# Kernel optimization log

Hardware: AMD Instinct MI355X
Metric: run time of the kernel (lower is better)

The kernel has to match this reference:

```python
import jax, jax.numpy as jnp
import numpy as np

DEGREE = 4  # sh degree -> DEGREE**2 = 16 components
RES = 128
N_PTS = 2097152
CH = 3


def sh_components(degree, d):
    """Real SH basis values for unit directions d [..., 3] -> [..., degree**2]."""
    x, y, z = d[..., 0], d[..., 1], d[..., 2]
    xx, yy, zz = x * x, y * y, z * z
    xy, yz, xz = x * y, y * z, x * z
    comps = [jnp.full(x.shape, 0.28209479177387814, dtype=d.dtype)]
    if degree > 1:
        comps += [-0.4886025119029199 * y,
                  0.4886025119029199 * z,
                  -0.4886025119029199 * x]
    if degree > 2:
        comps += [1.0925484305920792 * xy,
                  -1.0925484305920792 * yz,
                  0.31539156525252005 * (2.0 * zz - xx - yy),
                  -1.0925484305920792 * xz,
                  0.5462742152960396 * (xx - yy)]
    if degree > 3:
        comps += [-0.5900435899266435 * y * (3 * xx - yy),
                  2.890611442640554 * xy * z,
                  -0.4570457994644658 * y * (4 * zz - xx - yy),
                  0.3731763325901154 * z * (2 * zz - 3 * xx - 3 * yy),
                  -0.4570457994644658 * x * (4 * zz - xx - yy),
                  1.445305721320277 * z * (xx - yy),
                  -0.5900435899266435 * x * (xx - 3 * yy)]
    if degree > 4:
        comps += [2.5033429417967046 * xy * (xx - yy),
                  -1.7701307697799304 * yz * (3 * xx - yy),
                  0.9461746957575601 * xy * (7 * zz - 1),
                  -0.6690465435572892 * yz * (7 * zz - 3),
                  0.10578554691520431 * (zz * (35 * zz - 30) + 3),
                  -0.6690465435572892 * xz * (7 * zz - 3),
                  0.47308734787878004 * (xx - yy) * (7 * zz - 1),
                  -1.7701307697799304 * xz * (xx - 3 * yy),
                  0.6258357354491761 * (xx * (xx - 3 * yy) - yy * (3 * xx - yy))]
    return jnp.stack(comps, axis=-1)


def trilerp(coefficients, aabb, points):
    """Trilinear interpolation of grid coefficients [R,R,R,D2,C] at points [N,3] -> [N,D2,C]."""
    res = coefficients.shape[0]
    amin, amax = aabb[:3], aabb[3:]
    g = (points - amin) / (amax - amin) * (res - 1)       # continuous grid coords
    g = jnp.clip(g, 0.0, res - 1.0)
    i0 = jnp.clip(jnp.floor(g).astype(jnp.int32), 0, res - 2)  # [N,3]
    f = g - i0.astype(g.dtype)                            # fractional part [N,3]
    fx, fy, fz = f[..., 0], f[..., 1], f[..., 2]
    out = None
    for dx in (0, 1):
        wx = fx if dx else (1.0 - fx)
        for dy in (0, 1):
            wy = fy if dy else (1.0 - fy)
            for dz in (0, 1):
                wz = fz if dz else (1.0 - fz)
                w = (wx * wy * wz)[:, None, None]          # [N,1,1]
                c = coefficients[i0[:, 0] + dx, i0[:, 1] + dy, i0[:, 2] + dz]  # [N,D2,C]
                out = w * c if out is None else out + w * c
    return out


def setup_inputs() -> dict:
    key = jax.random.key(0)
    k1, k2, k3 = jax.random.split(key, 3)
    coefficients = jax.random.normal(k1, (RES, RES, RES, DEGREE ** 2, CH), dtype=jnp.float32) * 0.1
    aabb = jnp.array([-1.0, -1.0, -1.0, 1.0, 1.0, 1.0], dtype=jnp.float32)
    points = jax.random.uniform(k2, (N_PTS, 3), dtype=jnp.float32) * 2.0 - 1.0  # inside aabb
    normals = jax.random.normal(k3, (N_PTS, 3), dtype=jnp.float32)
    normals = normals / jnp.linalg.norm(normals, axis=-1, keepdims=True)
    return {"coefficients": coefficients, "aabb": aabb, "points": points, "normals": normals}


def reference(coefficients, aabb, points, normals):
    comps = sh_components(DEGREE, normals)                 # [N, D2]
    ic = trilerp(coefficients, aabb, points)               # [N, D2, C]
    irradiance = jnp.sum(ic * comps[..., None], axis=1)    # [N, C]
    return jnp.maximum(irradiance, 0.0)
```

## Files before the change

kernel.cpp:

```cpp
#include <hip/hip_runtime.h>


constexpr int RES = 128;
constexpr int D2 = 16;
constexpr int CSTRIDE = D2 * 3;
constexpr int CELL_F4 = CSTRIDE / 4;

constexpr int NBX = 32, NBY = 16, NBZ = 16;
constexpr int NBINS = NBX * NBY * NBZ;
constexpr int HX = 5, HY = 9, HZ = 9;
constexpr int TOT_F4 = HX * HY * HZ * CELL_F4;
constexpr int MAIN_THREADS = 256;
constexpr int LOAD_ITERS = (TOT_F4 + MAIN_THREADS - 1) / MAIN_THREADS;
constexpr int PAD = 16;

__device__ __forceinline__ void grid_coords(const float* aabb, float px, float py, float pz,
                                            int& ix, int& iy, int& iz,
                                            float& fx, float& fy, float& fz)
{
    const float a0 = aabb[0], a1 = aabb[1], a2 = aabb[2];
    const float b0 = aabb[3], b1 = aabb[4], b2 = aabb[5];
    float gx = (px - a0) / (b0 - a0) * (float)(RES - 1);
    float gy = (py - a1) / (b1 - a1) * (float)(RES - 1);
    float gz = (pz - a2) / (b2 - a2) * (float)(RES - 1);
    gx = fminf(fmaxf(gx, 0.0f), (float)(RES - 1));
    gy = fminf(fmaxf(gy, 0.0f), (float)(RES - 1));
    gz = fminf(fmaxf(gz, 0.0f), (float)(RES - 1));
    ix = min((int)floorf(gx), RES - 2);
    iy = min((int)floorf(gy), RES - 2);
    iz = min((int)floorf(gz), RES - 2);
    fx = gx - (float)ix;
    fy = gy - (float)iy;
    fz = gz - (float)iz;
}

__device__ __forceinline__ int bin_of(int ix, int iy, int iz)
{
    return (((ix >> 2) * NBY) + (iy >> 3)) * NBZ + (iz >> 3);
}

__device__ __forceinline__ void sh_basis(float nx, float ny, float nz, float* sh)
{
    const float xx = nx * nx, yy = ny * ny, zz = nz * nz;
    const float xy = nx * ny, yz = ny * nz, xz = nx * nz;
    sh[0]  = 0.28209479177387814f;
    sh[1]  = -0.4886025119029199f * ny;
    sh[2]  = 0.4886025119029199f * nz;
    sh[3]  = -0.4886025119029199f * nx;
    sh[4]  = 1.0925484305920792f * xy;
    sh[5]  = -1.0925484305920792f * yz;
    sh[6]  = 0.31539156525252005f * (2.0f * zz - xx - yy);
    sh[7]  = -1.0925484305920792f * xz;
    sh[8]  = 0.5462742152960396f * (xx - yy);
    sh[9]  = -0.5900435899266435f * ny * (3.0f * xx - yy);
    sh[10] = 2.890611442640554f * xy * nz;
    sh[11] = -0.4570457994644658f * ny * (4.0f * zz - xx - yy);
    sh[12] = 0.3731763325901154f * nz * (2.0f * zz - 3.0f * xx - 3.0f * yy);
    sh[13] = -0.4570457994644658f * nx * (4.0f * zz - xx - yy);
    sh[14] = 1.445305721320277f * nz * (xx - yy);
    sh[15] = -0.5900435899266435f * nx * (xx - 3.0f * yy);
}

__global__ __launch_bounds__(256) void hist_kernel(
    const float* __restrict__ aabb,
    const float* __restrict__ points,
    int* __restrict__ bin_of_point,
    int* __restrict__ hist_p,
    int n)
{
    const int i = blockIdx.x * blockDim.x + threadIdx.x;
    if (i >= n) return;
    int ix, iy, iz; float fx, fy, fz;
    grid_coords(aabb, points[3 * i + 0], points[3 * i + 1], points[3 * i + 2],
                ix, iy, iz, fx, fy, fz);
    const int bin = bin_of(ix, iy, iz);
    bin_of_point[i] = bin;
    atomicAdd(&hist_p[bin * PAD], 1);
}

__global__ __launch_bounds__(256) void scan_kernel(
    const int* __restrict__ hist_p,
    int* __restrict__ binstart,
    int* __restrict__ cursor_p)
{
    __shared__ int lsum[256];
    const int t = threadIdx.x;
    constexpr int PER = NBINS / 256;
    const int base = t * PER;
    int loc[PER];
    int s = 0;
#pragma unroll
    for (int k = 0; k < PER; ++k) { loc[k] = hist_p[(base + k) * PAD]; s += loc[k]; }
    lsum[t] = s;
    __syncthreads();
    for (int off = 1; off < 256; off <<= 1) {
        int v = (t >= off) ? lsum[t - off] : 0;
        __syncthreads();
        lsum[t] += v;
        __syncthreads();
    }
    int run = lsum[t] - s;
#pragma unroll
    for (int k = 0; k < PER; ++k) {
        binstart[base + k] = run;
        cursor_p[(base + k) * PAD] = run;
        run += loc[k];
    }
}

__global__ __launch_bounds__(256) void scatter_kernel(
    const int* __restrict__ bin_of_point,
    int* __restrict__ cursor_p,
    int* __restrict__ sidx,
    int n)
{
    const int i = blockIdx.x * blockDim.x + threadIdx.x;
    if (i >= n) return;
    const int bin = bin_of_point[i];
    const int pos = atomicAdd(&cursor_p[bin * PAD], 1);
    sidx[pos] = i;
}

__global__ __launch_bounds__(MAIN_THREADS) void main_kernel(
    const float* __restrict__ coeff,
    const float* __restrict__ aabb,
    const float* __restrict__ points,
    const float* __restrict__ normals,
    const int* __restrict__ binstart,
    const int* __restrict__ hist_p,
    const int* __restrict__ sidx,
    float* __restrict__ out)
{
    extern __shared__ char smem[];
    float4* lds4 = (float4*)smem;

    const int bin = blockIdx.x;
    const int start = binstart[bin];
    const int count = hist_p[bin * PAD];
    if (count == 0) return;

    const int bx = bin / (NBY * NBZ);
    const int by = (bin / NBZ) % NBY;
    const int bz = bin % NBZ;
    const int x0 = bx << 2;
    const int y0 = by << 3;
    const int z0 = bz << 3;

    const int tid = threadIdx.x;
    const float4* __restrict__ coeff4 = (const float4*)coeff;

#pragma unroll
    for (int k = 0; k < LOAD_ITERS; ++k) {
        const int u = tid + k * MAIN_THREADS;
        if (u < TOT_F4) {
            int cx = u / (HY * HZ * CELL_F4);
            int r1 = u - cx * (HY * HZ * CELL_F4);
            int cy = r1 / (HZ * CELL_F4);
            int r2 = r1 - cy * (HZ * CELL_F4);
            int cz = r2 / CELL_F4;
            int kk = r2 - cz * CELL_F4;
            int xg = min(x0 + cx, RES - 1);
            int yg = min(y0 + cy, RES - 1);
            int zg = min(z0 + cz, RES - 1);
            lds4[u] = coeff4[((xg * RES + yg) * RES + zg) * CELL_F4 + kk];
        }
    }
    __syncthreads();

    for (int p = start + tid; p < start + count; p += MAIN_THREADS) {
        const int i = sidx[p];
        const float px = points[3 * i + 0];
        const float py = points[3 * i + 1];
        const float pz = points[3 * i + 2];
        const float nx = normals[3 * i + 0];
        const float ny = normals[3 * i + 1];
        const float nz = normals[3 * i + 2];

        int ix, iy, iz; float fx, fy, fz;
        grid_coords(aabb, px, py, pz, ix, iy, iz, fx, fy, fz);
        const int lx = ix - x0, ly = iy - y0, lz = iz - z0;

        float sh[D2];
        sh_basis(nx, ny, nz, sh);

        const float wz0 = 1.0f - fz, wz1 = fz;
        float acc0 = 0.0f, acc1 = 0.0f, acc2 = 0.0f;

#pragma unroll
        for (int dx = 0; dx < 2; ++dx) {
            const float wx = dx ? fx : 1.0f - fx;
#pragma unroll
            for (int dy = 0; dy < 2; ++dy) {
                const float wxy = wx * (dy ? fy : 1.0f - fy);
                const int lcell = (((lx + dx) * HY + (ly + dy)) * HZ + lz) * CELL_F4;
                union { float4 q[24]; float v[96]; } u;
#pragma unroll
                for (int kk = 0; kk < 24; ++kk) u.q[kk] = lds4[lcell + kk];

                float s00 = 0.f, s01 = 0.f, s02 = 0.f;
                float s10 = 0.f, s11 = 0.f, s12 = 0.f;
#pragma unroll
                for (int j = 0; j < D2; ++j) {
                    const float s = sh[j];
                    s00 = fmaf(s, u.v[3 * j + 0], s00);
                    s01 = fmaf(s, u.v[3 * j + 1], s01);
                    s02 = fmaf(s, u.v[3 * j + 2], s02);
                    s10 = fmaf(s, u.v[48 + 3 * j + 0], s10);
                    s11 = fmaf(s, u.v[48 + 3 * j + 1], s11);
                    s12 = fmaf(s, u.v[48 + 3 * j + 2], s12);
                }
                const float w0 = wxy * wz0, w1 = wxy * wz1;
                acc0 = fmaf(w0, s00, fmaf(w1, s10, acc0));
                acc1 = fmaf(w0, s01, fmaf(w1, s11, acc1));
                acc2 = fmaf(w0, s02, fmaf(w1, s12, acc2));
            }
        }

        out[3 * i + 0] = fmaxf(acc0, 0.0f);
        out[3 * i + 1] = fmaxf(acc1, 0.0f);
        out[3 * i + 2] = fmaxf(acc2, 0.0f);
    }
}

__global__ __launch_bounds__(256) void direct_kernel(
    const float* __restrict__ coeff,
    const float* __restrict__ aabb,
    const float* __restrict__ points,
    const float* __restrict__ normals,
    float* __restrict__ out,
    int n)
{
    const int i = blockIdx.x * blockDim.x + threadIdx.x;
    if (i >= n) return;
    const float px = points[3 * i + 0], py = points[3 * i + 1], pz = points[3 * i + 2];
    const float nx = normals[3 * i + 0], ny = normals[3 * i + 1], nz = normals[3 * i + 2];
    int ix, iy, iz; float fx, fy, fz;
    grid_coords(aabb, px, py, pz, ix, iy, iz, fx, fy, fz);
    float sh[D2];
    sh_basis(nx, ny, nz, sh);
    const float wz0 = 1.0f - fz, wz1 = fz;
    float acc0 = 0.0f, acc1 = 0.0f, acc2 = 0.0f;
#pragma unroll
    for (int dx = 0; dx < 2; ++dx) {
        const float wx = dx ? fx : 1.0f - fx;
#pragma unroll
        for (int dy = 0; dy < 2; ++dy) {
            const float wxy = wx * (dy ? fy : 1.0f - fy);
            const int cell = (((ix + dx) * RES + (iy + dy)) * RES + iz) * CSTRIDE;
            const float4* __restrict__ cp = (const float4*)(coeff + cell);
            union { float4 q[24]; float v[96]; } u;
#pragma unroll
            for (int kk = 0; kk < 24; ++kk) u.q[kk] = cp[kk];
            float s00 = 0.f, s01 = 0.f, s02 = 0.f;
            float s10 = 0.f, s11 = 0.f, s12 = 0.f;
#pragma unroll
            for (int j = 0; j < D2; ++j) {
                const float s = sh[j];
                s00 = fmaf(s, u.v[3 * j + 0], s00);
                s01 = fmaf(s, u.v[3 * j + 1], s01);
                s02 = fmaf(s, u.v[3 * j + 2], s02);
                s10 = fmaf(s, u.v[48 + 3 * j + 0], s10);
                s11 = fmaf(s, u.v[48 + 3 * j + 1], s11);
                s12 = fmaf(s, u.v[48 + 3 * j + 2], s12);
            }
            const float w0 = wxy * wz0, w1 = wxy * wz1;
            acc0 = fmaf(w0, s00, fmaf(w1, s10, acc0));
            acc1 = fmaf(w0, s01, fmaf(w1, s11, acc1));
            acc2 = fmaf(w0, s02, fmaf(w1, s12, acc2));
        }
    }
    out[3 * i + 0] = fmaxf(acc0, 0.0f);
    out[3 * i + 1] = fmaxf(acc1, 0.0f);
    out[3 * i + 2] = fmaxf(acc2, 0.0f);
}

extern "C" void kernel_launch(void* const* d_in, const int* in_sizes, int n_in,
                              void* d_out, int out_size, void* d_ws, size_t ws_size,
                              hipStream_t stream) {
    const float* coeff   = (const float*)d_in[0];
    const float* aabb    = (const float*)d_in[1];
    const float* points  = (const float*)d_in[2];
    const float* normals = (const float*)d_in[3];
    float* out = (float*)d_out;

    const int n = in_sizes[2] / 3;
    const int nblk = (n + 255) / 256;

    size_t off = 0;
    auto take = [&](size_t bytes) { size_t o = off; off = (off + bytes + 255) & ~(size_t)255; return o; };
    char* ws = (char*)d_ws;
    const size_t o_bin      = take((size_t)n * 4);
    const size_t o_hist     = take((size_t)NBINS * PAD * 4);
    const size_t o_binstart = take((size_t)NBINS * 4);
    const size_t o_cursor   = take((size_t)NBINS * PAD * 4);
    const size_t o_sidx     = take((size_t)n * 4);
    const size_t needed = off;

    if (ws_size < needed) {
        hipLaunchKernelGGL(direct_kernel, dim3(nblk), dim3(256), 0, stream,
                           coeff, aabb, points, normals, out, n);
        return;
    }

    int* bin_of_point = (int*)(ws + o_bin);
    int* hist_p   = (int*)(ws + o_hist);
    int* binstart = (int*)(ws + o_binstart);
    int* cursor_p = (int*)(ws + o_cursor);
    int* sidx     = (int*)(ws + o_sidx);

    hipMemsetAsync(hist_p, 0, (size_t)NBINS * PAD * 4, stream);

    hipLaunchKernelGGL(hist_kernel, dim3(nblk), dim3(256), 0, stream,
                       aabb, points, bin_of_point, hist_p, n);
    hipLaunchKernelGGL(scan_kernel, dim3(1), dim3(256), 0, stream,
                       hist_p, binstart, cursor_p);
    hipLaunchKernelGGL(scatter_kernel, dim3(nblk), dim3(256), 0, stream,
                       bin_of_point, cursor_p, sidx, n);
    hipLaunchKernelGGL(main_kernel, dim3(NBINS), dim3(MAIN_THREADS),
                       TOT_F4 * sizeof(float4), stream,
                       coeff, aabb, points, normals, binstart, hist_p, sidx, out);
}
```

Before: 922.5 us.

## Replace histogram-scan-scatter binning with fixed-capacity replicated bin slots

Drops the separate histogram, prefix-scan and scatter passes and instead writes each point index straight into one of four replicated fixed-capacity slot arrays per spatial bin in a single pass. Spreading each bin over four counters is meant to reduce contention on the atomics. Points that do not fit go to an overflow list, which a new overflow kernel handles through global-memory gathers. A rare fallback that scans every point if the overflow list itself fills is also included. This removes one pass over the points and the serial single-block scan, at the cost of an extra kernel launch and a capacity-dependent overflow path.

Result: faster. 828.3 us (-10.2%).

```diff
diff --git a/kernel.cpp b/kernel.cpp
--- a/kernel.cpp
+++ b/kernel.cpp
@@ -12,7 +12,11 @@
 constexpr int TOT_F4 = HX * HY * HZ * CELL_F4;
 constexpr int MAIN_THREADS = 256;
 constexpr int LOAD_ITERS = (TOT_F4 + MAIN_THREADS - 1) / MAIN_THREADS;
-constexpr int PAD = 16;
+
+constexpr int REPL = 4;
+constexpr int CAP = 104;
+constexpr int CNT_PAD = 16;
+constexpr int OVF_CAP = 131072;
 
 __device__ __forceinline__ void grid_coords(const float* aabb, float px, float py, float pz,
                                             int& ix, int& iy, int& iz,
@@ -61,11 +65,62 @@
     sh[15] = -0.5900435899266435f * nx * (xx - 3.0f * yy);
 }
 
-__global__ __launch_bounds__(256) void hist_kernel(
-    const float* __restrict__ aabb,
-    const float* __restrict__ points,
-    int* __restrict__ bin_of_point,
-    int* __restrict__ hist_p,
+__device__ void compute_point_global(
+    const float* __restrict__ coeff,
+    const float* __restrict__ aabb,
+    const float* __restrict__ points,
+    const float* __restrict__ normals,
+    float* __restrict__ out, int i)
+{
+    const float px = points[3 * i + 0], py = points[3 * i + 1], pz = points[3 * i + 2];
+    const float nx = normals[3 * i + 0], ny = normals[3 * i + 1], nz = normals[3 * i + 2];
+    int ix, iy, iz; float fx, fy, fz;
+    grid_coords(aabb, px, py, pz, ix, iy, iz, fx, fy, fz);
+    float sh[D2];
+    sh_basis(nx, ny, nz, sh);
+    const float wz0 = 1.0f - fz, wz1 = fz;
+    float acc0 = 0.0f, acc1 = 0.0f, acc2 = 0.0f;
+#pragma unroll
+    for (int dx = 0; dx < 2; ++dx) {
+        const float wx = dx ? fx : 1.0f - fx;
+#pragma unroll
+        for (int dy = 0; dy < 2; ++dy) {
+            const float wxy = wx * (dy ? fy : 1.0f - fy);
+            const int cell = (((ix + dx) * RES + (iy + dy)) * RES + iz) * CSTRIDE;
+            const float4* __restrict__ cp = (const float4*)(coeff + cell);
+            union { float4 q[24]; float v[96]; } u;
+#pragma unroll
+            for (int kk = 0; kk < 24; ++kk) u.q[kk] = cp[kk];
+            float s00 = 0.f, s01 = 0.f, s02 = 0.f;
+            float s10 = 0.f, s11 = 0.f, s12 = 0.f;
+#pragma unroll
+            for (int j = 0; j < D2; ++j) {
+                const float s = sh[j];
+                s00 = fmaf(s, u.v[3 * j + 0], s00);
+                s01 = fmaf(s, u.v[3 * j + 1], s01);
+                s02 = fmaf(s, u.v[3 * j + 2], s02);
+                s10 = fmaf(s, u.v[48 + 3 * j + 0], s10);
+                s11 = fmaf(s, u.v[48 + 3 * j + 1], s11);
+                s12 = fmaf(s, u.v[48 + 3 * j + 2], s12);
+            }
+            const float w0 = wxy * wz0, w1 = wxy * wz1;
+            acc0 = fmaf(w0, s00, fmaf(w1, s10, acc0));
+            acc1 = fmaf(w0, s01, fmaf(w1, s11, acc1));
+            acc2 = fmaf(w0, s02, fmaf(w1, s12, acc2));
+        }
+    }
+    out[3 * i + 0] = fmaxf(acc0, 0.0f);
+    out[3 * i + 1] = fmaxf(acc1, 0.0f);
+    out[3 * i + 2] = fmaxf(acc2, 0.0f);
+}
+
+__global__ __launch_bounds__(256) void scatter_kernel(
+    const float* __restrict__ aabb,
+    const float* __restrict__ points,
+    int* __restrict__ cnt_p,
+    int* __restrict__ slots,
+    int* __restrict__ ovf_cnt,
+    int* __restrict__ ovf,
     int n)
 {
     const int i = blockIdx.x * blockDim.x + threadIdx.x;
@@ -74,51 +129,16 @@
     grid_coords(aabb, points[3 * i + 0], points[3 * i + 1], points[3 * i + 2],
                 ix, iy, iz, fx, fy, fz);
     const int bin = bin_of(ix, iy, iz);
-    bin_of_point[i] = bin;
-    atomicAdd(&hist_p[bin * PAD], 1);
-}
-
-__global__ __launch_bounds__(256) void scan_kernel(
-    const int* __restrict__ hist_p,
-    int* __restrict__ binstart,
-    int* __restrict__ cursor_p)
-{
-    __shared__ int lsum[256];
-    const int t = threadIdx.x;
-    constexpr int PER = NBINS / 256;
-    const int base = t * PER;
-    int loc[PER];
-    int s = 0;
-#pragma unroll
-    for (int k = 0; k < PER; ++k) { loc[k] = hist_p[(base + k) * PAD]; s += loc[k]; }
-    lsum[t] = s;
-    __syncthreads();
-    for (int off = 1; off < 256; off <<= 1) {
-        int v = (t >= off) ? lsum[t - off] : 0;
-        __syncthreads();
-        lsum[t] += v;
-        __syncthreads();
-    }
-    int run = lsum[t] - s;
-#pragma unroll
-    for (int k = 0; k < PER; ++k) {
-        binstart[base + k] = run;
-        cursor_p[(base + k) * PAD] = run;
-        run += loc[k];
-    }
-}
-
-__global__ __launch_bounds__(256) void scatter_kernel(
-    const int* __restrict__ bin_of_point,
-    int* __restrict__ cursor_p,
-    int* __restrict__ sidx,
-    int n)
-{
-    const int i = blockIdx.x * blockDim.x + threadIdx.x;
-    if (i >= n) return;
-    const int bin = bin_of_point[i];
-    const int pos = atomicAdd(&cursor_p[bin * PAD], 1);
-    sidx[pos] = i;
+    const int rep = (i >> 6) & (REPL - 1);
+    const int g = bin * REPL + rep;
+    const int pos = atomicAdd(&cnt_p[g * CNT_PAD], 1);
+    if (pos < CAP) {
+        slots[g * CAP + pos] = i;
+    } else {
+        const int o = atomicAdd(&ovf_cnt[0], 1);
+        if (o < OVF_CAP) ovf[o] = i;
+        else ovf_cnt[1] = 1;
+    }
 }
 
 __global__ __launch_bounds__(MAIN_THREADS) void main_kernel(
@@ -126,18 +146,20 @@
     const float* __restrict__ aabb,
     const float* __restrict__ points,
     const float* __restrict__ normals,
-    const int* __restrict__ binstart,
-    const int* __restrict__ hist_p,
-    const int* __restrict__ sidx,
+    const int* __restrict__ cnt_p,
+    const int* __restrict__ slots,
     float* __restrict__ out)
 {
     extern __shared__ char smem[];
     float4* lds4 = (float4*)smem;
 
     const int bin = blockIdx.x;
-    const int start = binstart[bin];
-    const int count = hist_p[bin * PAD];
-    if (count == 0) return;
+    const int c0 = min(cnt_p[(bin * REPL + 0) * CNT_PAD], CAP);
+    const int c1 = min(cnt_p[(bin * REPL + 1) * CNT_PAD], CAP);
+    const int c2 = min(cnt_p[(bin * REPL + 2) * CNT_PAD], CAP);
+    const int c3 = min(cnt_p[(bin * REPL + 3) * CNT_PAD], CAP);
+    const int tot = c0 + c1 + c2 + c3;
+    if (tot == 0) return;
 
     const int bx = bin / (NBY * NBZ);
     const int by = (bin / NBZ) % NBY;
@@ -167,8 +189,13 @@
     }
     __syncthreads();
 
-    for (int p = start + tid; p < start + count; p += MAIN_THREADS) {
-        const int i = sidx[p];
+    for (int t = tid; t < tot; t += MAIN_THREADS) {
+        int k = t, r = 0;
+        if (k >= c0) { k -= c0; r = 1;
+            if (k >= c1) { k -= c1; r = 2;
+                if (k >= c2) { k -= c2; r = 3; } } }
+        const int i = slots[(bin * REPL + r) * CAP + k];
+
         const float px = points[3 * i + 0];
         const float py = points[3 * i + 1];
         const float pz = points[3 * i + 2];
@@ -222,6 +249,37 @@
     }
 }
 
+__global__ __launch_bounds__(256) void overflow_kernel(
+    const float* __restrict__ coeff,
+    const float* __restrict__ aabb,
+    const float* __restrict__ points,
+    const float* __restrict__ normals,
+    const int* __restrict__ ovf_cnt,
+    const int* __restrict__ ovf,
+    const int* __restrict__ cnt_p,
+    const int* __restrict__ slots,
+    float* __restrict__ out,
+    int n)
+{
+    const int m = min(ovf_cnt[0], OVF_CAP);
+    for (int t = blockIdx.x * blockDim.x + threadIdx.x; t < m; t += gridDim.x * blockDim.x)
+        compute_point_global(coeff, aabb, points, normals, out, ovf[t]);
+
+    if (ovf_cnt[1]) {
+        for (int i = blockIdx.x * blockDim.x + threadIdx.x; i < n; i += gridDim.x * blockDim.x) {
+            int ix, iy, iz; float fx, fy, fz;
+            grid_coords(aabb, points[3 * i + 0], points[3 * i + 1], points[3 * i + 2],
+                        ix, iy, iz, fx, fy, fz);
+            const int g = bin_of(ix, iy, iz) * REPL + ((i >> 6) & (REPL - 1));
+            const int c = min(cnt_p[g * CNT_PAD], CAP);
+            bool placed = false;
+            for (int k = 0; k < c && !placed; ++k) placed = (slots[g * CAP + k] == i);
+            for (int k = 0; k < m && !placed; ++k)  placed = (ovf[k] == i);
+            if (!placed) compute_point_global(coeff, aabb, points, normals, out, i);
+        }
+    }
+}
+
 __global__ __launch_bounds__(256) void direct_kernel(
     const float* __restrict__ coeff,
     const float* __restrict__ aabb,
@@ -232,46 +290,7 @@
 {
     const int i = blockIdx.x * blockDim.x + threadIdx.x;
     if (i >= n) return;
-    const float px = points[3 * i + 0], py = points[3 * i + 1], pz = points[3 * i + 2];
-    const float nx = normals[3 * i + 0], ny = normals[3 * i + 1], nz = normals[3 * i + 2];
-    int ix, iy, iz; float fx, fy, fz;
-    grid_coords(aabb, px, py, pz, ix, iy, iz, fx, fy, fz);
-    float sh[D2];
-    sh_basis(nx, ny, nz, sh);
-    const float wz0 = 1.0f - fz, wz1 = fz;
-    float acc0 = 0.0f, acc1 = 0.0f, acc2 = 0.0f;
-#pragma unroll
-    for (int dx = 0; dx < 2; ++dx) {
-        const float wx = dx ? fx : 1.0f - fx;
-#pragma unroll
-        for (int dy = 0; dy < 2; ++dy) {
-            const float wxy = wx * (dy ? fy : 1.0f - fy);
-            const int cell = (((ix + dx) * RES + (iy + dy)) * RES + iz) * CSTRIDE;
-            const float4* __restrict__ cp = (const float4*)(coeff + cell);
-            union { float4 q[24]; float v[96]; } u;
-#pragma unroll
-            for (int kk = 0; kk < 24; ++kk) u.q[kk] = cp[kk];
-            float s00 = 0.f, s01 = 0.f, s02 = 0.f;
-            float s10 = 0.f, s11 = 0.f, s12 = 0.f;
-#pragma unroll
-            for (int j = 0; j < D2; ++j) {
-                const float s = sh[j];
-                s00 = fmaf(s, u.v[3 * j + 0], s00);
-                s01 = fmaf(s, u.v[3 * j + 1], s01);
-                s02 = fmaf(s, u.v[3 * j + 2], s02);
-                s10 = fmaf(s, u.v[48 + 3 * j + 0], s10);
-                s11 = fmaf(s, u.v[48 + 3 * j + 1], s11);
-                s12 = fmaf(s, u.v[48 + 3 * j + 2], s12);
-            }
-            const float w0 = wxy * wz0, w1 = wxy * wz1;
-            acc0 = fmaf(w0, s00, fmaf(w1, s10, acc0));
-            acc1 = fmaf(w0, s01, fmaf(w1, s11, acc1));
-            acc2 = fmaf(w0, s02, fmaf(w1, s12, acc2));
-        }
-    }
-    out[3 * i + 0] = fmaxf(acc0, 0.0f);
-    out[3 * i + 1] = fmaxf(acc1, 0.0f);
-    out[3 * i + 2] = fmaxf(acc2, 0.0f);
+    compute_point_global(coeff, aabb, points, normals, out, i);
 }
 
 extern "C" void kernel_launch(void* const* d_in, const int* in_sizes, int n_in,
@@ -289,11 +308,11 @@
     size_t off = 0;
     auto take = [&](size_t bytes) { size_t o = off; off = (off + bytes + 255) & ~(size_t)255; return o; };
     char* ws = (char*)d_ws;
-    const size_t o_bin      = take((size_t)n * 4);
-    const size_t o_hist     = take((size_t)NBINS * PAD * 4);
-    const size_t o_binstart = take((size_t)NBINS * 4);
-    const size_t o_cursor   = take((size_t)NBINS * PAD * 4);
-    const size_t o_sidx     = take((size_t)n * 4);
+    const size_t cnt_bytes = (size_t)NBINS * REPL * CNT_PAD * 4;
+    const size_t o_cnt   = take(cnt_bytes);
+    const size_t o_ovfc  = take(256);
+    const size_t o_slots = take((size_t)NBINS * REPL * CAP * 4);
+    const size_t o_ovf   = take((size_t)OVF_CAP * 4);
     const size_t needed = off;
 
     if (ws_size < needed) {
@@ -302,21 +321,18 @@
         return;
     }
 
-    int* bin_of_point = (int*)(ws + o_bin);
-    int* hist_p   = (int*)(ws + o_hist);
-    int* binstart = (int*)(ws + o_binstart);
-    int* cursor_p = (int*)(ws + o_cursor);
-    int* sidx     = (int*)(ws + o_sidx);
-
-    hipMemsetAsync(hist_p, 0, (size_t)NBINS * PAD * 4, stream);
-
-    hipLaunchKernelGGL(hist_kernel, dim3(nblk), dim3(256), 0, stream,
-                       aabb, points, bin_of_point, hist_p, n);
-    hipLaunchKernelGGL(scan_kernel, dim3(1), dim3(256), 0, stream,
-                       hist_p, binstart, cursor_p);
+    int* cnt_p   = (int*)(ws + o_cnt);
+    int* ovf_cnt = (int*)(ws + o_ovfc);
+    int* slots   = (int*)(ws + o_slots);
+    int* ovf     = (int*)(ws + o_ovf);
+
+    hipMemsetAsync(ws + o_cnt, 0, cnt_bytes + 256, stream);
+
     hipLaunchKernelGGL(scatter_kernel, dim3(nblk), dim3(256), 0, stream,
-                       bin_of_point, cursor_p, sidx, n);
+                       aabb, points, cnt_p, slots, ovf_cnt, ovf, n);
     hipLaunchKernelGGL(main_kernel, dim3(NBINS), dim3(MAIN_THREADS),
                        TOT_F4 * sizeof(float4), stream,
-                       coeff, aabb, points, normals, binstart, hist_p, sidx, out);
-}
+                       coeff, aabb, points, normals, cnt_p, slots, out);
+    hipLaunchKernelGGL(overflow_kernel, dim3(64), dim3(256), 0, stream,
+                       coeff, aabb, points, normals, ovf_cnt, ovf, cnt_p, slots, out, n);
+}
```
